# Kernel tuning notes

Hardware: AMD Instinct MI355X
Metric: run time of the kernel (lower is better)

## Reference

```python
import jax, jax.numpy as jnp
import numpy as np

N = 4096
D = 256
H = 8
HD = D // H
EPS = 1e-5
NEG = -1e9


def layer_norm(x, g, b):
    mu = jnp.mean(x, axis=-1, keepdims=True)
    var = jnp.mean(jnp.square(x - mu), axis=-1, keepdims=True)
    return (x - mu) * jax.lax.rsqrt(var + EPS) * g + b


def setup_inputs() -> dict:
    key = jax.random.key(0)
    ks = jax.random.split(key, 12)
    s = 1.0 / np.sqrt(D)
    inp = {
        "x": jax.random.normal(ks[0], (N, D), dtype=jnp.float32),
        "adj": jax.random.randint(ks[1], (N, N), 0, 2, dtype=jnp.int32),
        "Wq": jax.random.uniform(ks[2], (D, D), jnp.float32, -s, s),
        "Wk": jax.random.uniform(ks[3], (D, D), jnp.float32, -s, s),
        "Wv": jax.random.uniform(ks[4], (D, D), jnp.float32, -s, s),
        "bq": jnp.zeros((D,), jnp.float32),
        "bk": jnp.zeros((D,), jnp.float32),
        "bv": jnp.zeros((D,), jnp.float32),
        "Wo": jax.random.uniform(ks[5], (D, D), jnp.float32, -s, s),
        "bo": jnp.zeros((D,), jnp.float32),
        "g1": jnp.ones((D,), jnp.float32),
        "beta1": jnp.zeros((D,), jnp.float32),
        "W1": jax.random.uniform(ks[6], (2 * D, D), jnp.float32, -s, s),
        "b1": jnp.zeros((2 * D,), jnp.float32),
        "W2": jax.random.uniform(ks[7], (D, 2 * D), jnp.float32, -1.0 / np.sqrt(2 * D), 1.0 / np.sqrt(2 * D)),
        "b2": jnp.zeros((D,), jnp.float32),
        "g2": jnp.ones((D,), jnp.float32),
        "beta2": jnp.zeros((D,), jnp.float32),
    }
    return inp


def reference(x, adj, Wq, Wk, Wv, bq, bk, bv, Wo, bo, g1, beta1, W1, b1, W2, b2, g2, beta2):
    n = adj.shape[0]
    # allowed = adj + I > 0 ; attention only over neighbors + self-loop
    allowed = (adj + jnp.eye(n, dtype=adj.dtype)) > 0  # (n, n) bool

    q = (x @ Wq.T + bq).reshape(n, H, HD)
    k = (x @ Wk.T + bk).reshape(n, H, HD)
    v = (x @ Wv.T + bv).reshape(n, H, HD)

    scale = 1.0 / np.sqrt(HD)
    scores = jnp.einsum('nhd,mhd->hnm', q, k) * scale  # (H, n, n)
    scores = jnp.where(allowed[None, :, :], scores, NEG)
    attn = jax.nn.softmax(scores, axis=-1)
    o = jnp.einsum('hnm,mhd->nhd', attn, v).reshape(n, D)
    h = o @ Wo.T + bo

    x = layer_norm(x + h, g1, beta1)
    ffn = jax.nn.relu(x @ W1.T + b1) @ W2.T + b2
    x = layer_norm(x + ffn, g2, beta2)
    return x
```

## Files before the change

kernel.cpp:

```cpp
#include <hip/hip_runtime.h>
#include <hip/hip_bf16.h>

typedef __attribute__((ext_vector_type(4))) float f32x4;
typedef __attribute__((ext_vector_type(8))) short s16x8;

#define NROWS 4096
#define DMODEL 256
#define NHEAD 8
#define HDIM 32
#define PSTRIDE 72
#define OSTRIDE 33
#define M2C 24.0f
#define NM (NROWS * DMODEL)
#define SA_S 264
#define SH_S 268
#define SY_S 264
#define SR_S 520

__device__ __forceinline__ short bf16r(float f) {
    union { float f; unsigned u; } v; v.f = f;
    unsigned r = v.u + 0x7fffu + ((v.u >> 16) & 1u);
    return (short)(r >> 16);
}

__device__ __forceinline__ float fexp2(float x) {
    float r;
    asm("v_exp_f32 %0, %1" : "=v"(r) : "v"(x));
    return r;
}

__device__ __forceinline__ unsigned pk_bf16(float a, float b) {
#if __has_builtin(__builtin_amdgcn_cvt_pk_bf16_f32)
    typedef __bf16 bf2 __attribute__((ext_vector_type(2)));
    union { bf2 h; unsigned u; } c;
    c.h = __builtin_amdgcn_cvt_pk_bf16_f32(a, b);
    return c.u;
#else
    return (unsigned)(unsigned short)bf16r(a) | ((unsigned)(unsigned short)bf16r(b) << 16);
#endif
}

__device__ __forceinline__ s16x8 pack8(float4 a, float4 b) {
    s16x8 r;
    r[0] = bf16r(a.x); r[1] = bf16r(a.y); r[2] = bf16r(a.z); r[3] = bf16r(a.w);
    r[4] = bf16r(b.x); r[5] = bf16r(b.y); r[6] = bf16r(b.z); r[7] = bf16r(b.w);
    return r;
}

__global__ __launch_bounds__(256) void qkvprep_kernel(
        const float* __restrict__ X,
        const float* __restrict__ Wq, const float* __restrict__ Wk,
        const float* __restrict__ Wv,
        const float* __restrict__ bq, const float* __restrict__ bk,
        const float* __restrict__ bv,
        const int* __restrict__ adj, unsigned* __restrict__ mask,
        const float* __restrict__ Wo, const float* __restrict__ W1,
        const float* __restrict__ W2, short* __restrict__ Wb,
        short* __restrict__ Qb, short* __restrict__ Kb,
        short* __restrict__ Vswz) {
    __shared__ short sT[64 * 72];
    const int b = blockIdx.x;
    const int tid = threadIdx.x;
    const int lane = tid & 63;
    if (b < 768) {
        const int wv = tid >> 6;
        const int quad = lane >> 4, col = lane & 15;
        const int bx = b & 63, by = b >> 6;
        const int o0 = by * 64;
        const int z = o0 >> 8;
        const float* Wsrc = (z == 0) ? Wq : (z == 1 ? Wk : Wv);
        const float* bias = (z == 0) ? bq : (z == 1 ? bk : bv);
        const int ow0 = o0 & 255;
        const int n0 = bx * 64 + wv * 16;
        const float QSC = 0.25505653437397888f;

        f32x4 zero = {0.f, 0.f, 0.f, 0.f};
        f32x4 acc[4] = {zero, zero, zero, zero};
        const float* ap = X + (size_t)(n0 + col) * DMODEL + quad * 8;
#pragma unroll
        for (int k0 = 0; k0 < DMODEL; k0 += 32) {
            float4 a0 = *(const float4*)(ap + k0);
            float4 a1 = *(const float4*)(ap + k0 + 4);
            s16x8 af = pack8(a0, a1);
#pragma unroll
            for (int t = 0; t < 4; ++t) {
                const float* wp = Wsrc + (size_t)(ow0 + t * 16 + col) * DMODEL + quad * 8 + k0;
                s16x8 bf = pack8(*(const float4*)wp, *(const float4*)(wp + 4));
                acc[t] = __builtin_amdgcn_mfma_f32_16x16x32_bf16(af, bf, acc[t], 0, 0, 0);
            }
        }
        if (z != 2) {
#pragma unroll
            for (int t = 0; t < 4; ++t) {
                const int oo = ow0 + t * 16 + col;
                float bvv = bias[oo];
#pragma unroll
                for (int r = 0; r < 4; ++r) {
                    int n = n0 + quad * 4 + r;
                    float v = acc[t][r] + bvv;
                    if (z == 0) Qb[(size_t)n * DMODEL + oo] = bf16r(v * QSC);
                    else        Kb[(size_t)(oo >> 5) * NROWS * HDIM + (size_t)n * HDIM + (oo & 31)] = bf16r(v);
                }
            }
        } else {
#pragma unroll
            for (int t = 0; t < 4; ++t) {
                const int oot = t * 16 + col;
                float bvv = bias[ow0 + oot];
#pragma unroll
                for (int r = 0; r < 4; ++r) {
                    int nn = wv * 16 + quad * 4 + r;
                    sT[oot * 72 + nn] = bf16r(acc[t][r] + bvv);
                }
            }
            __syncthreads();
            const int f = tid >> 5;
            const int lh = f >> 2, hdh = (f >> 1) & 1, kh = f & 1;
            const int L0 = (tid & 31) * 2;
            const int hgl = (ow0 >> 5) + lh;
            short* dst = Vswz + (((size_t)(hgl * 64 + bx) * 4 + hdh * 2 + kh) * 512);
#pragma unroll
            for (int e = 0; e < 2; ++e) {
                int L = L0 + e;
                int hd_local = lh * 32 + hdh * 16 + (L & 15);
                int key_local = kh * 32 + ((L >> 4) * 8);
                s16x8 v = *(const s16x8*)&sT[hd_local * 72 + key_local];
                *(s16x8*)(dst + L * 8) = v;
            }
        }
    } else if (b < 2816) {
        const int waveid = (b - 768) * 4 + (tid >> 6);
        int4 av[8];
        int rows[8], segs[8];
#pragma unroll
        for (int i = 0; i < 8; ++i) {
            const int task = waveid + i * 8192;
            rows[i] = task >> 4; segs[i] = task & 15;
            av[i] = *(const int4*)(adj + (size_t)rows[i] * NROWS + segs[i] * 256 + lane * 4);
        }
#pragma unroll
        for (int i = 0; i < 8; ++i) {
            const int row = rows[i];
            const int c0 = segs[i] * 256 + lane * 4;
            unsigned nib = (unsigned)(av[i].x > 0 || c0 == row)
                         | ((unsigned)(av[i].y > 0 || c0 + 1 == row) << 1)
                         | ((unsigned)(av[i].z > 0 || c0 + 2 == row) << 2)
                         | ((unsigned)(av[i].w > 0 || c0 + 3 == row) << 3);
            unsigned v = nib << ((lane & 7) * 4);
            v |= __shfl_xor((int)v, 1, 64);
            v |= __shfl_xor((int)v, 2, 64);
            v |= __shfl_xor((int)v, 4, 64);
            if ((lane & 7) == 0)
                mask[row * 128 + segs[i] * 8 + (lane >> 3)] = v;
        }
    } else {
        int i = (b - 2816) * 2048 + tid * 8;
        const float* src; int off;
        if (i < 65536)       { src = Wo; off = i; }
        else if (i < 196608) { src = W1; off = i - 65536; }
        else                 { src = W2; off = i - 196608; }
        float4 a = *(const float4*)(src + off);
        float4 c = *(const float4*)(src + off + 4);
        *(s16x8*)(Wb + i) = pack8(a, c);
    }
}

__global__ __launch_bounds__(256) void attn_kernel(const short* __restrict__ Qb,
                                                   const short* __restrict__ Kb,
                                                   const short* __restrict__ Vswz,
                                                   const unsigned* __restrict__ mask,
                                                   float* __restrict__ Opart,
                                                   float* __restrict__ lpart) {
    __shared__ union {
        short sP[2][16 * PSTRIDE];
        float sO[HDIM][OSTRIDE];
    } u[4];
    __shared__ float sl[4][32];

    const int tid = threadIdx.x;
    const int wv = tid >> 6, lane = tid & 63;
    const int quad = lane >> 4, col = lane & 15;
    const int khalf = blockIdx.x & 1;
    const int h = (blockIdx.x >> 1) & 7;
    const int q0 = (blockIdx.x >> 4) * 32;
    const int kw = khalf * 2048 + wv * 512;

    s16x8 qf[2];
    qf[0] = *(const s16x8*)(Qb + (size_t)(q0 + col) * DMODEL + h * HDIM + quad * 8);
    qf[1] = *(const s16x8*)(Qb + (size_t)(q0 + 16 + col) * DMODEL + h * HDIM + quad * 8);

    const short* kp = Kb + (size_t)h * NROWS * HDIM + (size_t)(kw + col) * HDIM + quad * 8;
    const short* vbase = Vswz + ((size_t)(h * 64 + (kw >> 6)) * 4) * 512 + lane * 8;
    const unsigned* mp0 = mask + (size_t)(q0 + col) * 128 + (kw >> 5);
    const unsigned* mp1 = mp0 + 16 * 128;

    const short onev = (col == 0) ? (short)0x3F80 : (short)0;
    const s16x8 ones = {onev, onev, onev, onev, onev, onev, onev, onev};

    f32x4 zero = {0.f, 0.f, 0.f, 0.f};
    f32x4 acc[2][2] = {{zero, zero}, {zero, zero}};
    f32x4 lacc[2] = {zero, zero};
    const f32x4 cinit = {-M2C, -M2C, -M2C, -M2C};

#pragma unroll 2
    for (int it = 0; it < 8; ++it) {
        const short* k = kp + it * 64 * HDIM;
        s16x8 kf0 = *(const s16x8*)(k);
        s16x8 kf1 = *(const s16x8*)(k + 16 * HDIM);
        s16x8 kf2 = *(const s16x8*)(k + 32 * HDIM);
        s16x8 kf3 = *(const s16x8*)(k + 48 * HDIM);
        uint2 w0 = *(const uint2*)(mp0 + it * 2);
        uint2 w1 = *(const uint2*)(mp1 + it * 2);
        const short* vb = vbase + it * 4 * 512;
        s16x8 vf00 = *(const s16x8*)(vb);
        s16x8 vf01 = *(const s16x8*)(vb + 512);
        s16x8 vf10 = *(const s16x8*)(vb + 1024);
        s16x8 vf11 = *(const s16x8*)(vb + 1536);

#pragma unroll
        for (int qs = 0; qs < 2; ++qs) {
            unsigned wlo = (qs ? w1.x : w0.x) >> (quad * 4);
            unsigned whi = (qs ? w1.y : w0.y) >> (quad * 4);
            f32x4 st[4];
            st[0] = __builtin_amdgcn_mfma_f32_16x16x32_bf16(kf0, qf[qs], cinit, 0, 0, 0);
            st[1] = __builtin_amdgcn_mfma_f32_16x16x32_bf16(kf1, qf[qs], cinit, 0, 0, 0);
            st[2] = __builtin_amdgcn_mfma_f32_16x16x32_bf16(kf2, qf[qs], cinit, 0, 0, 0);
            st[3] = __builtin_amdgcn_mfma_f32_16x16x32_bf16(kf3, qf[qs], cinit, 0, 0, 0);

            float p[4][4];
#pragma unroll
            for (int t = 0; t < 4; ++t) {
                unsigned wm = (t < 2) ? wlo : whi;
#pragma unroll
                for (int r = 0; r < 4; ++r) {
                    float e = fexp2(st[t][r]);
                    bool ok = (wm & (1u << ((t & 1) * 16 + r))) != 0u;
                    p[t][r] = ok ? e : 0.f;
                }
            }

            short* pb = &u[wv].sP[qs][0];
#pragma unroll
            for (int t = 0; t < 4; ++t) {
                uint2 pr;
                pr.x = pk_bf16(p[t][0], p[t][1]);
                pr.y = pk_bf16(p[t][2], p[t][3]);
                *(uint2*)(pb + col * PSTRIDE + t * 16 + quad * 4) = pr;
            }
            s16x8 pb0 = *(const s16x8*)(pb + col * PSTRIDE + quad * 8);
            s16x8 pb1 = *(const s16x8*)(pb + col * PSTRIDE + 32 + quad * 8);

            acc[qs][0] = __builtin_amdgcn_mfma_f32_16x16x32_bf16(vf00, pb0, acc[qs][0], 0, 0, 0);
            acc[qs][0] = __builtin_amdgcn_mfma_f32_16x16x32_bf16(vf01, pb1, acc[qs][0], 0, 0, 0);
            acc[qs][1] = __builtin_amdgcn_mfma_f32_16x16x32_bf16(vf10, pb0, acc[qs][1], 0, 0, 0);
            acc[qs][1] = __builtin_amdgcn_mfma_f32_16x16x32_bf16(vf11, pb1, acc[qs][1], 0, 0, 0);
            lacc[qs] = __builtin_amdgcn_mfma_f32_16x16x32_bf16(ones, pb0, lacc[qs], 0, 0, 0);
            lacc[qs] = __builtin_amdgcn_mfma_f32_16x16x32_bf16(ones, pb1, lacc[qs], 0, 0, 0);
        }
    }

#pragma unroll
    for (int qs = 0; qs < 2; ++qs) {
        if (lane < 16) sl[wv][qs * 16 + col] = lacc[qs][0];
#pragma unroll
        for (int rr = 0; rr < 4; ++rr) {
            u[wv].sO[quad * 4 + rr][qs * 16 + col]      = acc[qs][0][rr];
            u[wv].sO[16 + quad * 4 + rr][qs * 16 + col] = acc[qs][1][rr];
        }
    }
    __syncthreads();

    const int q = tid >> 3, hd0 = (tid & 7) * 4;
    float l = sl[0][q] + sl[1][q] + sl[2][q] + sl[3][q];
    float4 ov;
    ov.x = u[0].sO[hd0][q]     + u[1].sO[hd0][q]     + u[2].sO[hd0][q]     + u[3].sO[hd0][q];
    ov.y = u[0].sO[hd0 + 1][q] + u[1].sO[hd0 + 1][q] + u[2].sO[hd0 + 1][q] + u[3].sO[hd0 + 1][q];
    ov.z = u[0].sO[hd0 + 2][q] + u[1].sO[hd0 + 2][q] + u[2].sO[hd0 + 2][q] + u[3].sO[hd0 + 2][q];
    ov.w = u[0].sO[hd0 + 3][q] + u[1].sO[hd0 + 3][q] + u[2].sO[hd0 + 3][q] + u[3].sO[hd0 + 3][q];
    *(float4*)(Opart + (size_t)khalf * NM + (size_t)(q0 + q) * DMODEL + h * HDIM + hd0) = ov;
    if ((tid & 7) == 0) lpart[khalf * NROWS * NHEAD + (q0 + q) * NHEAD + h] = l;
}

__global__ __launch_bounds__(512) void mega_kernel(
        const float* __restrict__ Opart, const float* __restrict__ lpart,
        const float* __restrict__ X,
        const short* __restrict__ Wob, const short* __restrict__ W1b,
        const short* __restrict__ W2b,
        const float* __restrict__ bo,
        const float* __restrict__ g1, const float* __restrict__ be1,
        const float* __restrict__ b1, const float* __restrict__ b2,
        const float* __restrict__ g2, const float* __restrict__ be2,
        float* __restrict__ out) {
    __shared__ union { short sA[16 * SA_S]; short sR[16 * SR_S]; } uu;
    __shared__ float sH[16 * SH_S];
    __shared__ short sY[16 * SY_S];

    const int tid = threadIdx.x;
    const int wv = tid >> 6, lane = tid & 63;
    const int quad = lane >> 4, col = lane & 15;
    const int n0 = blockIdx.x * 16;
    const int rr_ = tid >> 5, c8 = (tid & 31) * 8;
    const int n_ln = n0 + rr_;
    f32x4 zero = {0.f, 0.f, 0.f, 0.f};

    {
        const int head = c8 >> 5;
        float li = 1.f / (lpart[(size_t)n_ln * NHEAD + head] +
                          lpart[(size_t)NROWS * NHEAD + (size_t)n_ln * NHEAD + head]);
        const float* p0 = Opart + (size_t)n_ln * DMODEL + c8;
        const float* p1 = p0 + NM;
        float4 a0 = ((const float4*)p0)[0], a1 = ((const float4*)p0)[1];
        float4 b0 = ((const float4*)p1)[0], b1v = ((const float4*)p1)[1];
        s16x8 w;
        *((unsigned*)&w + 0) = pk_bf16((a0.x + b0.x) * li, (a0.y + b0.y) * li);
        *((unsigned*)&w + 1) = pk_bf16((a0.z + b0.z) * li, (a0.w + b0.w) * li);
        *((unsigned*)&w + 2) = pk_bf16((a1.x + b1v.x) * li, (a1.y + b1v.y) * li);
        *((unsigned*)&w + 3) = pk_bf16((a1.z + b1v.z) * li, (a1.w + b1v.w) * li);
        *(s16x8*)&uu.sA[rr_ * SA_S + c8] = w;
    }
    __syncthreads();

    {
        const int o0 = wv * 32;
        f32x4 acc[2] = {zero, zero};
#pragma unroll
        for (int k0 = 0; k0 < DMODEL; k0 += 32) {
            s16x8 af = *(const s16x8*)&uu.sA[col * SA_S + k0 + quad * 8];
#pragma unroll
            for (int t = 0; t < 2; ++t) {
                s16x8 bf = *(const s16x8*)(Wob + (size_t)(o0 + t * 16 + col) * DMODEL + k0 + quad * 8);
                acc[t] = __builtin_amdgcn_mfma_f32_16x16x32_bf16(af, bf, acc[t], 0, 0, 0);
            }
        }
#pragma unroll
        for (int t = 0; t < 2; ++t) {
            int o = o0 + t * 16 + col;
            float bv = bo[o];
#pragma unroll
            for (int r = 0; r < 4; ++r)
                sH[(quad * 4 + r) * SH_S + o] = acc[t][r] + bv;
        }
    }
    __syncthreads();

    float y1v[8];
    {
        const float* xp = X + (size_t)n_ln * DMODEL + c8;
        float v[8];
        float s = 0.f;
#pragma unroll
        for (int j = 0; j < 2; ++j) {
            float4 xv = ((const float4*)xp)[j];
            float4 hv = *(const float4*)&sH[rr_ * SH_S + c8 + j * 4];
            v[j * 4 + 0] = xv.x + hv.x; v[j * 4 + 1] = xv.y + hv.y;
            v[j * 4 + 2] = xv.z + hv.z; v[j * 4 + 3] = xv.w + hv.w;
            s += v[j * 4] + v[j * 4 + 1] + v[j * 4 + 2] + v[j * 4 + 3];
        }
#pragma unroll
        for (int m = 1; m < 32; m <<= 1) s += __shfl_xor(s, m, 64);
        float mean = s * (1.f / 256.f);
        float q = 0.f;
#pragma unroll
        for (int i = 0; i < 8; ++i) { v[i] -= mean; q += v[i] * v[i]; }
#pragma unroll
        for (int m = 1; m < 32; m <<= 1) q += __shfl_xor(q, m, 64);
        float rstd = rsqrtf(q * (1.f / 256.f) + 1e-5f);
        const float* gp = g1 + c8;
        const float* bp = be1 + c8;
        s16x8 w;
#pragma unroll
        for (int j = 0; j < 2; ++j) {
            float4 gv = ((const float4*)gp)[j];
            float4 bev = ((const float4*)bp)[j];
            float a0 = v[j * 4 + 0] * rstd * gv.x + bev.x;
            float a1 = v[j * 4 + 1] * rstd * gv.y + bev.y;
            float a2 = v[j * 4 + 2] * rstd * gv.z + bev.z;
            float a3 = v[j * 4 + 3] * rstd * gv.w + bev.w;
            y1v[j * 4 + 0] = a0; y1v[j * 4 + 1] = a1;
            y1v[j * 4 + 2] = a2; y1v[j * 4 + 3] = a3;
            *((unsigned*)&w + j * 2 + 0) = pk_bf16(a0, a1);
            *((unsigned*)&w + j * 2 + 1) = pk_bf16(a2, a3);
        }
        *(s16x8*)&sY[rr_ * SY_S + c8] = w;
    }
    __syncthreads();

    {
        const int o0 = wv * 64;
        f32x4 acc[4] = {zero, zero, zero, zero};
#pragma unroll
        for (int k0 = 0; k0 < DMODEL; k0 += 32) {
            s16x8 af = *(const s16x8*)&sY[col * SY_S + k0 + quad * 8];
#pragma unroll
            for (int t = 0; t < 4; ++t) {
                s16x8 bf = *(const s16x8*)(W1b + (size_t)(o0 + t * 16 + col) * DMODEL + k0 + quad * 8);
                acc[t] = __builtin_amdgcn_mfma_f32_16x16x32_bf16(af, bf, acc[t], 0, 0, 0);
            }
        }
#pragma unroll
        for (int t = 0; t < 4; ++t) {
            int o = o0 + t * 16 + col;
            float bv = b1[o];
#pragma unroll
            for (int r = 0; r < 4; ++r)
                uu.sR[(quad * 4 + r) * SR_S + o] = bf16r(fmaxf(acc[t][r] + bv, 0.f));
        }
    }
    __syncthreads();

    {
        const int o0 = wv * 32;
        f32x4 acc[2] = {zero, zero};
#pragma unroll
        for (int k0 = 0; k0 < 512; k0 += 32) {
            s16x8 af = *(const s16x8*)&uu.sR[col * SR_S + k0 + quad * 8];
#pragma unroll
            for (int t = 0; t < 2; ++t) {
                s16x8 bf = *(const s16x8*)(W2b + (size_t)(o0 + t * 16 + col) * 512 + k0 + quad * 8);
                acc[t] = __builtin_amdgcn_mfma_f32_16x16x32_bf16(af, bf, acc[t], 0, 0, 0);
            }
        }
#pragma unroll
        for (int t = 0; t < 2; ++t) {
            int o = o0 + t * 16 + col;
            float bv = b2[o];
#pragma unroll
            for (int r = 0; r < 4; ++r)
                sH[(quad * 4 + r) * SH_S + o] = acc[t][r] + bv;
        }
    }
    __syncthreads();

    {
        float v[8];
        float s = 0.f;
#pragma unroll
        for (int j = 0; j < 2; ++j) {
            float4 hv = *(const float4*)&sH[rr_ * SH_S + c8 + j * 4];
            v[j * 4 + 0] = y1v[j * 4 + 0] + hv.x; v[j * 4 + 1] = y1v[j * 4 + 1] + hv.y;
            v[j * 4 + 2] = y1v[j * 4 + 2] + hv.z; v[j * 4 + 3] = y1v[j * 4 + 3] + hv.w;
            s += v[j * 4] + v[j * 4 + 1] + v[j * 4 + 2] + v[j * 4 + 3];
        }
#pragma unroll
        for (int m = 1; m < 32; m <<= 1) s += __shfl_xor(s, m, 64);
        float mean = s * (1.f / 256.f);
        float q = 0.f;
#pragma unroll
        for (int i = 0; i < 8; ++i) { v[i] -= mean; q += v[i] * v[i]; }
#pragma unroll
        for (int m = 1; m < 32; m <<= 1) q += __shfl_xor(q, m, 64);
        float rstd = rsqrtf(q * (1.f / 256.f) + 1e-5f);
        const float* gp = g2 + c8;
        const float* bp = be2 + c8;
        float* op = out + (size_t)n_ln * DMODEL + c8;
#pragma unroll
        for (int j = 0; j < 2; ++j) {
            float4 gv = ((const float4*)gp)[j];
            float4 bev = ((const float4*)bp)[j];
            float4 y;
            y.x = v[j * 4 + 0] * rstd * gv.x + bev.x;
            y.y = v[j * 4 + 1] * rstd * gv.y + bev.y;
            y.z = v[j * 4 + 2] * rstd * gv.z + bev.z;
            y.w = v[j * 4 + 3] * rstd * gv.w + bev.w;
            ((float4*)op)[j] = y;
        }
    }
}

extern "C" void kernel_launch(void* const* d_in, const int* in_sizes, int n_in,
                              void* d_out, int out_size, void* d_ws, size_t ws_size,
                              hipStream_t stream) {
    const float* x   = (const float*)d_in[0];
    const int*   adj = (const int*)d_in[1];
    const float* Wq  = (const float*)d_in[2];
    const float* Wk  = (const float*)d_in[3];
    const float* Wv  = (const float*)d_in[4];
    const float* bq  = (const float*)d_in[5];
    const float* bk  = (const float*)d_in[6];
    const float* bv  = (const float*)d_in[7];
    const float* Wo  = (const float*)d_in[8];
    const float* bo  = (const float*)d_in[9];
    const float* g1  = (const float*)d_in[10];
    const float* be1 = (const float*)d_in[11];
    const float* W1  = (const float*)d_in[12];
    const float* b1  = (const float*)d_in[13];
    const float* W2  = (const float*)d_in[14];
    const float* b2  = (const float*)d_in[15];
    const float* g2  = (const float*)d_in[16];
    const float* be2 = (const float*)d_in[17];
    float* out = (float*)d_out;

    char* p = (char*)d_ws;
    unsigned* mask = (unsigned*)p; p += (size_t)NROWS * 128 * 4;
    short* Wb    = (short*)p;      p += (size_t)327680 * 2;
    short* Qb    = (short*)p;      p += (size_t)NM * 2;
    short* Kb    = (short*)p;      p += (size_t)NM * 2;
    short* Vswz  = (short*)p;      p += (size_t)NM * 2;
    float* Opart = (float*)p;      p += (size_t)2 * NM * 4;
    float* lpart = (float*)p;      p += (size_t)2 * NROWS * NHEAD * 4;

    qkvprep_kernel<<<dim3(2976), dim3(256), 0, stream>>>(
        x, Wq, Wk, Wv, bq, bk, bv, adj, mask, Wo, W1, W2, Wb, Qb, Kb, Vswz);
    attn_kernel<<<dim3(2048), dim3(256), 0, stream>>>(Qb, Kb, Vswz, mask, Opart, lpart);
    mega_kernel<<<dim3(256), dim3(512), 0, stream>>>(
        Opart, lpart, x, Wb, Wb + 65536, Wb + 196608,
        bo, g1, be1, b1, b2, g2, be2, out);
}
```

Before: 227.9 us.

## Drop split-K attention partials; normalize and emit bf16 output in attention kernel

The attention kernel no longer splits the key range across two blocks. Each block now covers all 4096 keys, with each of its four waves taking 1024 keys, so the grid halves to 1024 blocks. The block normalizes by the row sum and writes a bf16 head output directly. This removes the fp32 partial O/l buffers, their write and re-read, and the combine stage plus one barrier in the downstream kernel, which now reads bf16 A-fragments straight from global. The trade-off is less parallelism per attention launch (1024 blocks instead of 2048) and longer per-block loops.

```diff
diff --git a/kernel.cpp b/kernel.cpp
--- a/kernel.cpp
+++ b/kernel.cpp
@@ -12,7 +12,6 @@
 #define OSTRIDE 33
 #define M2C 24.0f
 #define NM (NROWS * DMODEL)
-#define SA_S 264
 #define SH_S 268
 #define SY_S 264
 #define SR_S 520
@@ -169,8 +168,7 @@
                                                    const short* __restrict__ Kb,
                                                    const short* __restrict__ Vswz,
                                                    const unsigned* __restrict__ mask,
-                                                   float* __restrict__ Opart,
-                                                   float* __restrict__ lpart) {
+                                                   short* __restrict__ Om) {
     __shared__ union {
         short sP[2][16 * PSTRIDE];
         float sO[HDIM][OSTRIDE];
@@ -180,10 +178,9 @@
     const int tid = threadIdx.x;
     const int wv = tid >> 6, lane = tid & 63;
     const int quad = lane >> 4, col = lane & 15;
-    const int khalf = blockIdx.x & 1;
-    const int h = (blockIdx.x >> 1) & 7;
-    const int q0 = (blockIdx.x >> 4) * 32;
-    const int kw = khalf * 2048 + wv * 512;
+    const int h = blockIdx.x & 7;
+    const int q0 = (blockIdx.x >> 3) * 32;
+    const int kw = wv * 1024;
 
     s16x8 qf[2];
     qf[0] = *(const s16x8*)(Qb + (size_t)(q0 + col) * DMODEL + h * HDIM + quad * 8);
@@ -203,7 +200,7 @@
     const f32x4 cinit = {-M2C, -M2C, -M2C, -M2C};
 
 #pragma unroll 2
-    for (int it = 0; it < 8; ++it) {
+    for (int it = 0; it < 16; ++it) {
         const short* k = kp + it * 64 * HDIM;
         s16x8 kf0 = *(const s16x8*)(k);
         s16x8 kf1 = *(const s16x8*)(k + 16 * HDIM);
@@ -272,17 +269,20 @@
 
     const int q = tid >> 3, hd0 = (tid & 7) * 4;
     float l = sl[0][q] + sl[1][q] + sl[2][q] + sl[3][q];
+    float inv = 1.f / l;
     float4 ov;
     ov.x = u[0].sO[hd0][q]     + u[1].sO[hd0][q]     + u[2].sO[hd0][q]     + u[3].sO[hd0][q];
     ov.y = u[0].sO[hd0 + 1][q] + u[1].sO[hd0 + 1][q] + u[2].sO[hd0 + 1][q] + u[3].sO[hd0 + 1][q];
     ov.z = u[0].sO[hd0 + 2][q] + u[1].sO[hd0 + 2][q] + u[2].sO[hd0 + 2][q] + u[3].sO[hd0 + 2][q];
     ov.w = u[0].sO[hd0 + 3][q] + u[1].sO[hd0 + 3][q] + u[2].sO[hd0 + 3][q] + u[3].sO[hd0 + 3][q];
-    *(float4*)(Opart + (size_t)khalf * NM + (size_t)(q0 + q) * DMODEL + h * HDIM + hd0) = ov;
-    if ((tid & 7) == 0) lpart[khalf * NROWS * NHEAD + (q0 + q) * NHEAD + h] = l;
+    uint2 ob;
+    ob.x = pk_bf16(ov.x * inv, ov.y * inv);
+    ob.y = pk_bf16(ov.z * inv, ov.w * inv);
+    *(uint2*)(Om + (size_t)(q0 + q) * DMODEL + h * HDIM + hd0) = ob;
 }
 
 __global__ __launch_bounds__(512) void mega_kernel(
-        const float* __restrict__ Opart, const float* __restrict__ lpart,
+        const short* __restrict__ Omb,
         const float* __restrict__ X,
         const short* __restrict__ Wob, const short* __restrict__ W1b,
         const short* __restrict__ W2b,
@@ -291,7 +291,7 @@
         const float* __restrict__ b1, const float* __restrict__ b2,
         const float* __restrict__ g2, const float* __restrict__ be2,
         float* __restrict__ out) {
-    __shared__ union { short sA[16 * SA_S]; short sR[16 * SR_S]; } uu;
+    __shared__ short sR[16 * SR_S];
     __shared__ float sH[16 * SH_S];
     __shared__ short sY[16 * SY_S];
 
@@ -304,28 +304,11 @@
     f32x4 zero = {0.f, 0.f, 0.f, 0.f};
 
     {
-        const int head = c8 >> 5;
-        float li = 1.f / (lpart[(size_t)n_ln * NHEAD + head] +
-                          lpart[(size_t)NROWS * NHEAD + (size_t)n_ln * NHEAD + head]);
-        const float* p0 = Opart + (size_t)n_ln * DMODEL + c8;
-        const float* p1 = p0 + NM;
-        float4 a0 = ((const float4*)p0)[0], a1 = ((const float4*)p0)[1];
-        float4 b0 = ((const float4*)p1)[0], b1v = ((const float4*)p1)[1];
-        s16x8 w;
-        *((unsigned*)&w + 0) = pk_bf16((a0.x + b0.x) * li, (a0.y + b0.y) * li);
-        *((unsigned*)&w + 1) = pk_bf16((a0.z + b0.z) * li, (a0.w + b0.w) * li);
-        *((unsigned*)&w + 2) = pk_bf16((a1.x + b1v.x) * li, (a1.y + b1v.y) * li);
-        *((unsigned*)&w + 3) = pk_bf16((a1.z + b1v.z) * li, (a1.w + b1v.w) * li);
-        *(s16x8*)&uu.sA[rr_ * SA_S + c8] = w;
-    }
-    __syncthreads();
-
-    {
         const int o0 = wv * 32;
         f32x4 acc[2] = {zero, zero};
 #pragma unroll
         for (int k0 = 0; k0 < DMODEL; k0 += 32) {
-            s16x8 af = *(const s16x8*)&uu.sA[col * SA_S + k0 + quad * 8];
+            s16x8 af = *(const s16x8*)(Omb + (size_t)(n0 + col) * DMODEL + k0 + quad * 8);
 #pragma unroll
             for (int t = 0; t < 2; ++t) {
                 s16x8 bf = *(const s16x8*)(Wob + (size_t)(o0 + t * 16 + col) * DMODEL + k0 + quad * 8);
@@ -403,7 +386,7 @@
             float bv = b1[o];
 #pragma unroll
             for (int r = 0; r < 4; ++r)
-                uu.sR[(quad * 4 + r) * SR_S + o] = bf16r(fmaxf(acc[t][r] + bv, 0.f));
+                sR[(quad * 4 + r) * SR_S + o] = bf16r(fmaxf(acc[t][r] + bv, 0.f));
         }
     }
     __syncthreads();
@@ -413,7 +396,7 @@
         f32x4 acc[2] = {zero, zero};
 #pragma unroll
         for (int k0 = 0; k0 < 512; k0 += 32) {
-            s16x8 af = *(const s16x8*)&uu.sR[col * SR_S + k0 + quad * 8];
+            s16x8 af = *(const s16x8*)&sR[col * SR_S + k0 + quad * 8];
 #pragma unroll
             for (int t = 0; t < 2; ++t) {
                 s16x8 bf = *(const s16x8*)(W2b + (size_t)(o0 + t * 16 + col) * 512 + k0 + quad * 8);
@@ -492,17 +475,16 @@
 
     char* p = (char*)d_ws;
     unsigned* mask = (unsigned*)p; p += (size_t)NROWS * 128 * 4;
-    short* Wb    = (short*)p;      p += (size_t)327680 * 2;
-    short* Qb    = (short*)p;      p += (size_t)NM * 2;
-    short* Kb    = (short*)p;      p += (size_t)NM * 2;
-    short* Vswz  = (short*)p;      p += (size_t)NM * 2;
-    float* Opart = (float*)p;      p += (size_t)2 * NM * 4;
-    float* lpart = (float*)p;      p += (size_t)2 * NROWS * NHEAD * 4;
+    short* Wb   = (short*)p;       p += (size_t)327680 * 2;
+    short* Qb   = (short*)p;       p += (size_t)NM * 2;
+    short* Kb   = (short*)p;       p += (size_t)NM * 2;
+    short* Vswz = (short*)p;       p += (size_t)NM * 2;
+    short* Omb  = (short*)p;       p += (size_t)NM * 2;
 
     qkvprep_kernel<<<dim3(2976), dim3(256), 0, stream>>>(
         x, Wq, Wk, Wv, bq, bk, bv, adj, mask, Wo, W1, W2, Wb, Qb, Kb, Vswz);
-    attn_kernel<<<dim3(2048), dim3(256), 0, stream>>>(Qb, Kb, Vswz, mask, Opart, lpart);
+    attn_kernel<<<dim3(1024), dim3(256), 0, stream>>>(Qb, Kb, Vswz, mask, Omb);
     mega_kernel<<<dim3(256), dim3(512), 0, stream>>>(
-        Opart, lpart, x, Wb, Wb + 65536, Wb + 196608,
+        Omb, x, Wb, Wb + 65536, Wb + 196608,
         bo, g1, be1, b1, b2, g2, be2, out);
 }
```

After: 225.4 us. No clear change (-1.1%).
